# Optimization experiments

Hardware: AMD Instinct MI355X
Metric: run time of the kernel (lower is better)

The kernel has to match this reference:

```python
import jax, jax.numpy as jnp
import numpy as np

B, L, D, H = 2, 2048, 2048, 16
Dh = D // H
THETA = 500000.0


def _init_rope(dim, seq_len, n_heads):
    # Returns freqs_cis of shape (1, seq_len, 1, head_dim//2, 2) -> [..., 0]=cos, [..., 1]=sin
    hd = dim // n_heads
    inv_freqs = 1.0 / (THETA ** (jnp.arange(0, hd, 2, dtype=jnp.float32) / hd))
    t = jnp.arange(seq_len, dtype=jnp.float32)
    freqs = jnp.outer(t, inv_freqs).astype(jnp.float32)  # (L, hd/2)
    fc = jnp.stack([jnp.cos(freqs)[None, :, None, :],
                    jnp.sin(freqs)[None, :, None, :]], axis=3)  # (1, L, 1, 2, hd/2)
    return fc.transpose(0, 1, 2, 4, 3)  # (1, L, 1, hd/2, 2)


def _apply_rope(q, k, freqs_cis):
    def rotate(x):
        x2 = x.reshape(*x.shape[:-1], -1, 2)  # (B, L, H, Dh/2, 2)
        f = freqs_cis[:, :x.shape[1]]
        cos, sin = f[..., 0], f[..., 1]
        r = jnp.stack([x2[..., 0] * cos - x2[..., 1] * sin,
                       x2[..., 1] * cos + x2[..., 0] * sin], axis=-1)
        return r.reshape(*x.shape)
    return rotate(q), rotate(k)


def setup_inputs() -> dict:
    key = jax.random.key(0)
    kx, kq, kk, kv, ko = jax.random.split(key, 5)
    scale = 1.0 / np.sqrt(D)
    x = jax.random.normal(kx, (B, L, D), dtype=jnp.float32)
    Wq = jax.random.normal(kq, (D, H, Dh), dtype=jnp.float32) * scale
    Wk = jax.random.normal(kk, (D, H, Dh), dtype=jnp.float32) * scale
    Wv = jax.random.normal(kv, (D, H, Dh), dtype=jnp.float32) * scale
    Wo = jax.random.normal(ko, (D, D), dtype=jnp.float32) * scale
    return {"x": x, "Wq": Wq, "Wk": Wk, "Wv": Wv, "Wo": Wo}


def reference(x, Wq, Wk, Wv, Wo):
    freqs_cis = _init_rope(D, L, H)
    q = jnp.einsum('bld,dhk->blhk', x, Wq)  # (B, L, H, Dh)
    k = jnp.einsum('bld,dhk->blhk', x, Wk)
    v = jnp.einsum('bld,dhk->blhk', x, Wv)
    q, k = _apply_rope(q, k, freqs_cis)
    q = q / (Dh ** 0.5)
    att = jnp.einsum('bqhd,bkhd->bhqk', q, k)  # (B, H, L, L)
    Lq = x.shape[1]
    mask = jnp.tril(jnp.ones((1, 1, Lq, Lq), dtype=jnp.bool_))
    neg_inf = jnp.finfo(jnp.float32).min
    att = jnp.where(mask, att, neg_inf)
    att = jax.nn.softmax(att, axis=-1)
    out = jnp.einsum('bhqk,bkhd->bqhd', att, v)  # (B, L, H, Dh)
    out = out.reshape(x.shape)
    return jnp.einsum('bld,de->ble', out, Wo)
```

## Files before the change

### kernel.cpp

```cpp
#include <hip/hip_runtime.h>

typedef unsigned short u16;
typedef unsigned int u32;

#define Bb 2
#define Lc 2048
#define Dc 2048
#define Hc 16
#define DhC 128

typedef __bf16 bf16x8 __attribute__((ext_vector_type(8)));
typedef float f32x4 __attribute__((ext_vector_type(4)));

__device__ __forceinline__ u16 f2b(float f) {
  u32 u = __float_as_uint(f);
  u32 r = (u + 0x7fffu + ((u >> 16) & 1u)) >> 16;
  return (u16)r;
}
__device__ __forceinline__ float b2f(u16 u) {
  return __uint_as_float(((u32)u) << 16);
}

__device__ __forceinline__ void gll16(const void* g, void* l) {
  __builtin_amdgcn_global_load_lds(
      (const __attribute__((address_space(1))) u32*)g,
      (__attribute__((address_space(3))) u32*)l, 16, 0, 0);
}

__global__ __launch_bounds__(256) void sniff_dtype(const u16* __restrict__ x,
                                                   int* __restrict__ flag) {
  __shared__ int bad;
  if (threadIdx.x == 0) bad = 0;
  __syncthreads();
  int local = 0;
  for (int i = threadIdx.x; i < 65536; i += 256) {
    float v = fabsf(b2f(x[i]));
    if (!(v < 1000.f)) local = 1;
  }
  if (local) atomicOr(&bad, 1);
  __syncthreads();
  if (threadIdx.x == 0) *flag = bad;
}

__global__ __launch_bounds__(256) void conv_x(const void* __restrict__ in,
                                              u16* __restrict__ out,
                                              const int* __restrict__ flag) {
  const int f32 = *flag;
  const int i0 = (blockIdx.x * 256 + threadIdx.x) * 4;
  if (f32) {
    const float* p = (const float*)in;
#pragma unroll
    for (int j = 0; j < 4; j++) out[i0 + j] = f2b(p[i0 + j]);
  } else {
    const u16* p = (const u16*)in;
#pragma unroll
    for (int j = 0; j < 4; j++) out[i0 + j] = p[i0 + j];
  }
}

__global__ __launch_bounds__(256) void transpose2d_conv(const void* __restrict__ in,
                                                        u16* __restrict__ out,
                                                        const int* __restrict__ flag) {
  __shared__ __align__(16) u16 tile[64][65];
  const int f32 = *flag;
  const int r0 = blockIdx.y * 64, c0 = blockIdx.x * 64;
  const int tc = threadIdx.x & 63, tr4 = threadIdx.x >> 6;
#pragma unroll
  for (int p = 0; p < 16; p++) {
    int r = tr4 + p * 4;
    size_t idx = (size_t)(r0 + r) * 2048 + c0 + tc;
    tile[r][tc] = f32 ? f2b(((const float*)in)[idx]) : ((const u16*)in)[idx];
  }
  __syncthreads();
#pragma unroll
  for (int p = 0; p < 16; p++) {
    int rr = tr4 + p * 4;
    out[(size_t)(c0 + rr) * 2048 + r0 + tc] = tile[tc][rr];
  }
}

template <typename OutT>
__device__ __forceinline__ void gemm_bt_core(const u16* __restrict__ A,
                                             const u16* __restrict__ Bt,
                                             OutT* __restrict__ C) {
  constexpr int K = 2048, N = 2048;
  __shared__ __align__(16) u16 As[128 * 64];
  __shared__ __align__(16) u16 Bs[128 * 64];
  const int tid = threadIdx.x;
  const int lane = tid & 63, wid = tid >> 6;
  const int wm = (wid >> 1) * 64, wn = (wid & 1) * 64;
  const int m0 = blockIdx.x * 128, n0 = blockIdx.y * 128;
  const int quad = lane >> 4, l15 = lane & 15;
  const int sw = l15 & 7;

  const f32x4 fz = {0.f, 0.f, 0.f, 0.f};
  f32x4 acc[4][4];
#pragma unroll
  for (int i = 0; i < 4; i++)
#pragma unroll
    for (int j = 0; j < 4; j++) acc[i][j] = fz;

  const int srl = (lane >> 3);
  const int ssl = lane & 7;

  for (int k0 = 0; k0 < K; k0 += 64) {
#pragma unroll
    for (int p = 0; p < 4; p++) {
      const int r = p * 32 + wid * 8 + srl;
      const int c = ssl ^ (r & 7);
      u16* lb = As + (p * 256 + wid * 64) * 8;
      gll16(A + (size_t)(m0 + r) * K + k0 + c * 8, lb);
    }
#pragma unroll
    for (int p = 0; p < 4; p++) {
      const int r = p * 32 + wid * 8 + srl;
      const int c = ssl ^ (r & 7);
      u16* lb = Bs + (p * 256 + wid * 64) * 8;
      gll16(Bt + (size_t)(n0 + r) * K + k0 + c * 8, lb);
    }
    __syncthreads();
#pragma unroll
    for (int ks = 0; ks < 2; ks++) {
      bf16x8 af[4], bfr[4];
#pragma unroll
      for (int t = 0; t < 4; t++) {
        const int cc = ((ks * 4 + quad) ^ sw) * 8;
        af[t]  = *(const bf16x8*)(&As[(wm + t * 16 + l15) * 64 + cc]);
        bfr[t] = *(const bf16x8*)(&Bs[(wn + t * 16 + l15) * 64 + cc]);
      }
#pragma unroll
      for (int mt = 0; mt < 4; mt++)
#pragma unroll
        for (int nt = 0; nt < 4; nt++)
          acc[mt][nt] = __builtin_amdgcn_mfma_f32_16x16x32_bf16(af[mt], bfr[nt], acc[mt][nt], 0, 0, 0);
    }
    __syncthreads();
  }
#pragma unroll
  for (int mt = 0; mt < 4; mt++)
#pragma unroll
    for (int nt = 0; nt < 4; nt++) {
      int col = n0 + wn + nt * 16 + l15;
#pragma unroll
      for (int r = 0; r < 4; r++) {
        int row = m0 + wm + mt * 16 + quad * 4 + r;
        float v = acc[mt][nt][r];
        if constexpr (sizeof(OutT) == 2)
          C[(size_t)row * N + col] = f2b(v);
        else
          C[(size_t)row * N + col] = v;
      }
    }
}

__global__ __launch_bounds__(256) void gemm_bt(const u16* __restrict__ A,
                                               const u16* __restrict__ Bt,
                                               u16* __restrict__ C) {
  gemm_bt_core<u16>(A, Bt, C);
}
__global__ __launch_bounds__(256) void gemm_bt_f32(const u16* __restrict__ A,
                                                   const u16* __restrict__ Bt,
                                                   float* __restrict__ C) {
  gemm_bt_core<float>(A, Bt, C);
}

__global__ __launch_bounds__(256) void transpose_v_k(const u16* __restrict__ V,
                                                     u16* __restrict__ Vt) {
  __shared__ __align__(16) u16 tile[64][65];
  const int z = blockIdx.z;
  const int b = z >> 4, h = z & 15;
  const int l0 = blockIdx.y * 64, d0 = blockIdx.x * 64;
  const int tc = threadIdx.x & 63, tr4 = threadIdx.x >> 6;
#pragma unroll
  for (int p = 0; p < 16; p++) {
    int l = tr4 + p * 4;
    tile[l][tc] = V[(size_t)((b * Lc + l0 + l) * Hc + h) * DhC + d0 + tc];
  }
  __syncthreads();
#pragma unroll
  for (int p = 0; p < 16; p++) {
    int dd = tr4 + p * 4;
    Vt[((size_t)z * DhC + d0 + dd) * Lc + l0 + tc] = tile[tc][dd];
  }
}

__global__ __launch_bounds__(256) void rope_qk(u16* __restrict__ Q, u16* __restrict__ K) {
  const int idx = blockIdx.x * 256 + threadIdx.x;
  const int j = idx & 63;
  const int l = (idx >> 10) & 2047;
  const float inv = expf(-0.2050369278f * (float)j);
  const float ang = (float)l * inv;
  float s, c;
  sincosf(ang, &s, &c);
  const size_t off = (size_t)idx * 2;
  const float q0 = b2f(Q[off]), q1 = b2f(Q[off + 1]);
  const float k0 = b2f(K[off]), k1 = b2f(K[off + 1]);
  const float sc = 0.08838834764f;
  Q[off]     = f2b((q0 * c - q1 * s) * sc);
  Q[off + 1] = f2b((q1 * c + q0 * s) * sc);
  K[off]     = f2b(k0 * c - k1 * s);
  K[off + 1] = f2b(k1 * c + k0 * s);
}

#define NEGBIG (-3.0e30f)
__global__ __launch_bounds__(256) void flash_attn(const u16* __restrict__ Q,
                                                  const u16* __restrict__ Kg,
                                                  const u16* __restrict__ Vt,
                                                  u16* __restrict__ O) {
  __shared__ __align__(16) u16 Ks[2][64 * 128];
  __shared__ __align__(16) u16 Vs[2][128 * 64];
  __shared__ __align__(16) u16 Ps[4][16][72];
  const int tid = threadIdx.x;
  const int lane = tid & 63, w = tid >> 6;
  const int quad = lane >> 4, l15 = lane & 15;
  const int qt = (int)gridDim.x - 1 - (int)blockIdx.x;
  const int bh = blockIdx.y;
  const int b = bh >> 4, h = bh & 15;
  const int q0 = qt * 64;
  const int qrow = q0 + w * 16 + l15;

  const int krl = lane >> 4, ksl = lane & 15;
  const int vrl = lane >> 3, vsl = lane & 7;

  bf16x8 aq[4];
  const u16* qptr = Q + ((size_t)(b * Lc + qrow) * Hc + h) * DhC + quad * 8;
#pragma unroll
  for (int ks = 0; ks < 4; ks++) aq[ks] = *(const bf16x8*)(qptr + ks * 32);

  {
#pragma unroll
    for (int p = 0; p < 4; p++) {
      const int r = p * 16 + w * 4 + krl;
      const int c = ksl ^ (r & 15);
      gll16(Kg + ((size_t)(b * Lc + r) * Hc + h) * DhC + c * 8,
            &Ks[0][(p * 256 + w * 64) * 8]);
    }
#pragma unroll
    for (int p = 0; p < 4; p++) {
      const int r = p * 32 + w * 8 + vrl;
      const int c = vsl ^ (r & 7);
      gll16(Vt + ((size_t)bh * DhC + r) * Lc + c * 8,
            &Vs[0][(p * 256 + w * 64) * 8]);
    }
  }

  const f32x4 fz = {0.f, 0.f, 0.f, 0.f};
  f32x4 o[8];
#pragma unroll
  for (int f = 0; f < 8; f++) o[f] = fz;
  float mrow[4], lrow[4];
#pragma unroll
  for (int r = 0; r < 4; r++) { mrow[r] = NEGBIG; lrow[r] = 0.f; }

  __syncthreads();

  for (int kvt = 0; kvt <= qt; kvt++) {
    const int cur = kvt & 1;
    const u16* Ksc = Ks[cur];
    const u16* Vsc = Vs[cur];

    if (kvt < qt) {
      const int nv0 = (kvt + 1) * 64;
      const int nxt = cur ^ 1;
#pragma unroll
      for (int p = 0; p < 4; p++) {
        const int r = p * 16 + w * 4 + krl;
        const int c = ksl ^ (r & 15);
        gll16(Kg + ((size_t)(b * Lc + nv0 + r) * Hc + h) * DhC + c * 8,
              &Ks[nxt][(p * 256 + w * 64) * 8]);
      }
#pragma unroll
      for (int p = 0; p < 4; p++) {
        const int r = p * 32 + w * 8 + vrl;
        const int c = vsl ^ (r & 7);
        gll16(Vt + ((size_t)bh * DhC + r) * Lc + nv0 + c * 8,
              &Vs[nxt][(p * 256 + w * 64) * 8]);
      }
    }

    f32x4 s[4];
#pragma unroll
    for (int ct = 0; ct < 4; ct++) s[ct] = fz;
#pragma unroll
    for (int ks = 0; ks < 4; ks++) {
#pragma unroll
      for (int ct = 0; ct < 4; ct++) {
        bf16x8 bk = *(const bf16x8*)(
            &Ksc[(ct * 16 + l15) * 128 + (((ks << 2) + quad) ^ l15) * 8]);
        s[ct] = __builtin_amdgcn_mfma_f32_16x16x32_bf16(aq[ks], bk, s[ct], 0, 0, 0);
      }
    }

    if (kvt == qt) {
      const int kv0 = kvt * 64;
#pragma unroll
      for (int ct = 0; ct < 4; ct++) {
        int kvc = kv0 + ct * 16 + l15;
#pragma unroll
        for (int r = 0; r < 4; r++) {
          int qr = q0 + w * 16 + quad * 4 + r;
          if (kvc > qr) s[ct][r] = NEGBIG;
        }
      }
    }

    float mnew[4], alpha[4];
#pragma unroll
    for (int r = 0; r < 4; r++) {
      float mx = fmaxf(fmaxf(s[0][r], s[1][r]), fmaxf(s[2][r], s[3][r]));
#pragma unroll
      for (int off = 1; off < 16; off <<= 1) mx = fmaxf(mx, __shfl_xor(mx, off, 64));
      mnew[r] = fmaxf(mrow[r], mx);
      alpha[r] = __expf(mrow[r] - mnew[r]);
      mrow[r] = mnew[r];
    }
    float psum[4] = {0.f, 0.f, 0.f, 0.f};
#pragma unroll
    for (int ct = 0; ct < 4; ct++) {
#pragma unroll
      for (int r = 0; r < 4; r++) {
        float p = __expf(s[ct][r] - mnew[r]);
        s[ct][r] = p;
        psum[r] += p;
      }
    }
#pragma unroll
    for (int r = 0; r < 4; r++) {
#pragma unroll
      for (int off = 1; off < 16; off <<= 1) psum[r] += __shfl_xor(psum[r], off, 64);
      lrow[r] = lrow[r] * alpha[r] + psum[r];
    }
#pragma unroll
    for (int f = 0; f < 8; f++)
#pragma unroll
      for (int r = 0; r < 4; r++) o[f][r] *= alpha[r];

#pragma unroll
    for (int ct = 0; ct < 4; ct++)
#pragma unroll
      for (int r = 0; r < 4; r++)
        Ps[w][quad * 4 + r][ct * 16 + l15] = f2b(s[ct][r]);

#pragma unroll
    for (int ks = 0; ks < 2; ks++) {
      bf16x8 ap = *(const bf16x8*)(&Ps[w][l15][ks * 32 + quad * 8]);
#pragma unroll
      for (int f = 0; f < 8; f++) {
        bf16x8 bv = *(const bf16x8*)(
            &Vsc[(f * 16 + l15) * 64 + ((((ks << 2) + quad)) ^ (l15 & 7)) * 8]);
        o[f] = __builtin_amdgcn_mfma_f32_16x16x32_bf16(ap, bv, o[f], 0, 0, 0);
      }
    }

    __syncthreads();
  }

#pragma unroll
  for (int f = 0; f < 8; f++) {
    int d = f * 16 + l15;
#pragma unroll
    for (int r = 0; r < 4; r++) {
      int qr = q0 + w * 16 + quad * 4 + r;
      O[((size_t)(b * Lc + qr) * Hc + h) * DhC + d] = f2b(o[f][r] / lrow[r]);
    }
  }
}

extern "C" void kernel_launch(void* const* d_in, const int* in_sizes, int n_in,
                              void* d_out, int out_size, void* d_ws, size_t ws_size,
                              hipStream_t stream) {
  const void* x  = d_in[0];
  const void* Wq = d_in[1];
  const void* Wk = d_in[2];
  const void* Wv = d_in[3];
  const void* Wo = d_in[4];
  float* out = (float*)d_out;

  char* w = (char*)d_ws;
  const size_t WSZ = (size_t)2048 * 2048;
  const size_t XSZ = (size_t)Bb * Lc * Dc;
  int* flag = (int*)w;
  u16* WT  = (u16*)(w + 256);
  u16* xc  = WT + WSZ;
  u16* Qb  = xc + XSZ;
  u16* Kb  = Qb + XSZ;
  u16* Vb  = Kb + XSZ;
  u16* Vtb = xc;
  u16* Ob  = Vb;

  sniff_dtype<<<1, 256, 0, stream>>>((const u16*)x, flag);
  conv_x<<<(int)(XSZ / 1024), 256, 0, stream>>>(x, xc, flag);

  dim3 tgrid(32, 32);
  dim3 ggrid(32, 16);

  transpose2d_conv<<<tgrid, 256, 0, stream>>>(Wq, WT, flag);
  gemm_bt<<<ggrid, 256, 0, stream>>>(xc, WT, Qb);
  transpose2d_conv<<<tgrid, 256, 0, stream>>>(Wk, WT, flag);
  gemm_bt<<<ggrid, 256, 0, stream>>>(xc, WT, Kb);
  transpose2d_conv<<<tgrid, 256, 0, stream>>>(Wv, WT, flag);
  gemm_bt<<<ggrid, 256, 0, stream>>>(xc, WT, Vb);

  rope_qk<<<(Bb * Lc * Hc * 64) / 256, 256, 0, stream>>>(Qb, Kb);

  dim3 vgrid(2, 32, 32);
  transpose_v_k<<<vgrid, 256, 0, stream>>>(Vb, Vtb);

  dim3 fgrid(32, 32);
  flash_attn<<<fgrid, 256, 0, stream>>>(Qb, Kb, Vtb, Ob);

  transpose2d_conv<<<tgrid, 256, 0, stream>>>(Wo, WT, flag);
  gemm_bt_f32<<<ggrid, 256, 0, stream>>>(Ob, WT, out);
}
```

Measured before the change: 590.6 us.

## Rewrite flash attention with 32x32 MFMA, 128-row Q tiles and register P

Rewrites the flash attention kernel so each block handles 128 query rows and each wave 32 rows, switching to 32x32x16 MFMA with S computed transposed (K as A operand). P goes from accumulator to A-operand layout through lane shuffles and packed bf16 converts, so the LDS round trip is gone. It adds a lazy rescale that skips the output correction when the running max grows by no more than 8, s_setprio around the MFMA blocks, causal-balanced tile ordering across heads, and a launch-bounds occupancy hint. The aim is higher MFMA throughput, more K/V reuse per tile and less softmax and LDS overhead, at the cost of more registers and idle waves on diagonal tiles.

```diff
diff --git a/kernel.cpp b/kernel.cpp
--- a/kernel.cpp
+++ b/kernel.cpp
@@ -11,6 +11,7 @@
 
 typedef __bf16 bf16x8 __attribute__((ext_vector_type(8)));
 typedef float f32x4 __attribute__((ext_vector_type(4)));
+typedef float f32x16 __attribute__((ext_vector_type(16)));
 
 __device__ __forceinline__ u16 f2b(float f) {
   u32 u = __float_as_uint(f);
@@ -19,6 +20,12 @@
 }
 __device__ __forceinline__ float b2f(u16 u) {
   return __uint_as_float(((u32)u) << 16);
+}
+
+__device__ __forceinline__ u32 cvtpk(float lo, float hi) {
+  u32 r;
+  asm("v_cvt_pk_bf16_f32 %0, %1, %2" : "=v"(r) : "v"(lo), "v"(hi));
+  return r;
 }
 
 __device__ __forceinline__ void gll16(const void* g, void* l) {
@@ -203,29 +210,31 @@
 }
 
 #define NEGBIG (-3.0e30f)
-__global__ __launch_bounds__(256) void flash_attn(const u16* __restrict__ Q,
-                                                  const u16* __restrict__ Kg,
-                                                  const u16* __restrict__ Vt,
-                                                  u16* __restrict__ O) {
+__global__ __launch_bounds__(256, 2) void flash_attn(const u16* __restrict__ Q,
+                                                     const u16* __restrict__ Kg,
+                                                     const u16* __restrict__ Vt,
+                                                     u16* __restrict__ O) {
   __shared__ __align__(16) u16 Ks[2][64 * 128];
   __shared__ __align__(16) u16 Vs[2][128 * 64];
-  __shared__ __align__(16) u16 Ps[4][16][72];
   const int tid = threadIdx.x;
   const int lane = tid & 63, w = tid >> 6;
-  const int quad = lane >> 4, l15 = lane & 15;
-  const int qt = (int)gridDim.x - 1 - (int)blockIdx.x;
+  const int l31 = lane & 31, hib = lane >> 5;
   const int bh = blockIdx.y;
   const int b = bh >> 4, h = bh & 15;
-  const int q0 = qt * 64;
-  const int qrow = q0 + w * 16 + l15;
+  const int qt = (bh & 16) ? (int)blockIdx.x : (15 - (int)blockIdx.x);
+  const int q0 = qt * 128;
+  const int qw0 = q0 + w * 32;
+  const int nkv = 2 * qt + 2;
 
   const int krl = lane >> 4, ksl = lane & 15;
   const int vrl = lane >> 3, vsl = lane & 7;
 
-  bf16x8 aq[4];
-  const u16* qptr = Q + ((size_t)(b * Lc + qrow) * Hc + h) * DhC + quad * 8;
-#pragma unroll
-  for (int ks = 0; ks < 4; ks++) aq[ks] = *(const bf16x8*)(qptr + ks * 32);
+  bf16x8 qf[8];
+  {
+    const u16* qptr = Q + ((size_t)(b * Lc + qw0 + l31) * Hc + h) * DhC + 8 * hib;
+#pragma unroll
+    for (int s = 0; s < 8; s++) qf[s] = *(const bf16x8*)(qptr + s * 16);
+  }
 
   {
 #pragma unroll
@@ -244,22 +253,19 @@
     }
   }
 
-  const f32x4 fz = {0.f, 0.f, 0.f, 0.f};
-  f32x4 o[8];
-#pragma unroll
-  for (int f = 0; f < 8; f++) o[f] = fz;
-  float mrow[4], lrow[4];
-#pragma unroll
-  for (int r = 0; r < 4; r++) { mrow[r] = NEGBIG; lrow[r] = 0.f; }
+  f32x16 o[4];
+#pragma unroll
+  for (int dt = 0; dt < 4; dt++) o[dt] = (f32x16)0.0f;
+  float mrow = NEGBIG, lrow = 0.f;
 
   __syncthreads();
 
-  for (int kvt = 0; kvt <= qt; kvt++) {
+  for (int kvt = 0; kvt < nkv; kvt++) {
     const int cur = kvt & 1;
     const u16* Ksc = Ks[cur];
     const u16* Vsc = Vs[cur];
 
-    if (kvt < qt) {
+    if (kvt + 1 < nkv) {
       const int nv0 = (kvt + 1) * 64;
       const int nxt = cur ^ 1;
 #pragma unroll
@@ -278,91 +284,125 @@
       }
     }
 
-    f32x4 s[4];
-#pragma unroll
-    for (int ct = 0; ct < 4; ct++) s[ct] = fz;
-#pragma unroll
-    for (int ks = 0; ks < 4; ks++) {
-#pragma unroll
-      for (int ct = 0; ct < 4; ct++) {
-        bf16x8 bk = *(const bf16x8*)(
-            &Ksc[(ct * 16 + l15) * 128 + (((ks << 2) + quad) ^ l15) * 8]);
-        s[ct] = __builtin_amdgcn_mfma_f32_16x16x32_bf16(aq[ks], bk, s[ct], 0, 0, 0);
-      }
-    }
-
-    if (kvt == qt) {
-      const int kv0 = kvt * 64;
-#pragma unroll
-      for (int ct = 0; ct < 4; ct++) {
-        int kvc = kv0 + ct * 16 + l15;
-#pragma unroll
-        for (int r = 0; r < 4; r++) {
-          int qr = q0 + w * 16 + quad * 4 + r;
-          if (kvc > qr) s[ct][r] = NEGBIG;
+    const int kv0 = kvt * 64;
+    const bool active = (kv0 <= qw0 + 31);
+    if (active) {
+      f32x16 s0 = (f32x16)0.0f, s1 = (f32x16)0.0f;
+      __builtin_amdgcn_s_setprio(1);
+#pragma unroll
+      for (int s = 0; s < 8; s++) {
+        const int ch = ((2 * s + hib) ^ (l31 & 15)) * 8;
+        bf16x8 k0 = *(const bf16x8*)(&Ksc[l31 * 128 + ch]);
+        bf16x8 k1 = *(const bf16x8*)(&Ksc[(32 + l31) * 128 + ch]);
+        s0 = __builtin_amdgcn_mfma_f32_32x32x16_bf16(k0, qf[s], s0, 0, 0, 0);
+        s1 = __builtin_amdgcn_mfma_f32_32x32x16_bf16(k1, qf[s], s1, 0, 0, 0);
+      }
+      __builtin_amdgcn_s_setprio(0);
+
+      if (kv0 + 63 > qw0) {
+        const int qg = qw0 + l31;
+#pragma unroll
+        for (int r = 0; r < 16; r++) {
+          const int cr = (r & 3) + 8 * (r >> 2) + 4 * hib;
+          if (kv0 + cr > qg) s0[r] = NEGBIG;
+          if (kv0 + 32 + cr > qg) s1[r] = NEGBIG;
         }
       }
-    }
-
-    float mnew[4], alpha[4];
-#pragma unroll
-    for (int r = 0; r < 4; r++) {
-      float mx = fmaxf(fmaxf(s[0][r], s[1][r]), fmaxf(s[2][r], s[3][r]));
-#pragma unroll
-      for (int off = 1; off < 16; off <<= 1) mx = fmaxf(mx, __shfl_xor(mx, off, 64));
-      mnew[r] = fmaxf(mrow[r], mx);
-      alpha[r] = __expf(mrow[r] - mnew[r]);
-      mrow[r] = mnew[r];
-    }
-    float psum[4] = {0.f, 0.f, 0.f, 0.f};
-#pragma unroll
-    for (int ct = 0; ct < 4; ct++) {
-#pragma unroll
-      for (int r = 0; r < 4; r++) {
-        float p = __expf(s[ct][r] - mnew[r]);
-        s[ct][r] = p;
-        psum[r] += p;
-      }
-    }
-#pragma unroll
-    for (int r = 0; r < 4; r++) {
-#pragma unroll
-      for (int off = 1; off < 16; off <<= 1) psum[r] += __shfl_xor(psum[r], off, 64);
-      lrow[r] = lrow[r] * alpha[r] + psum[r];
-    }
-#pragma unroll
-    for (int f = 0; f < 8; f++)
-#pragma unroll
-      for (int r = 0; r < 4; r++) o[f][r] *= alpha[r];
-
-#pragma unroll
-    for (int ct = 0; ct < 4; ct++)
-#pragma unroll
-      for (int r = 0; r < 4; r++)
-        Ps[w][quad * 4 + r][ct * 16 + l15] = f2b(s[ct][r]);
-
-#pragma unroll
-    for (int ks = 0; ks < 2; ks++) {
-      bf16x8 ap = *(const bf16x8*)(&Ps[w][l15][ks * 32 + quad * 8]);
-#pragma unroll
-      for (int f = 0; f < 8; f++) {
-        bf16x8 bv = *(const bf16x8*)(
-            &Vsc[(f * 16 + l15) * 64 + ((((ks << 2) + quad)) ^ (l15 & 7)) * 8]);
-        o[f] = __builtin_amdgcn_mfma_f32_16x16x32_bf16(ap, bv, o[f], 0, 0, 0);
-      }
+
+      float mx;
+      {
+        float a[8];
+#pragma unroll
+        for (int i = 0; i < 8; i++)
+          a[i] = fmaxf(fmaxf(s0[i], s0[i + 8]), fmaxf(s1[i], s1[i + 8]));
+        float b0 = fmaxf(a[0], a[4]), b1 = fmaxf(a[1], a[5]);
+        float b2 = fmaxf(a[2], a[6]), b3 = fmaxf(a[3], a[7]);
+        mx = fmaxf(fmaxf(b0, b1), fmaxf(b2, b3));
+      }
+      mx = fmaxf(mx, __shfl_xor(mx, 32, 64));
+
+      if (!__all(mx - mrow <= 8.f)) {
+        const float mnew = fmaxf(mrow, mx);
+        const float al = __expf(mrow - mnew);
+#pragma unroll
+        for (int dt = 0; dt < 4; dt++)
+#pragma unroll
+          for (int e = 0; e < 16; e++) o[dt][e] *= al;
+        lrow *= al;
+        mrow = mnew;
+      }
+
+#pragma unroll
+      for (int i = 0; i < 16; i++) {
+        s0[i] = __expf(s0[i] - mrow);
+        s1[i] = __expf(s1[i] - mrow);
+      }
+      float sm;
+      {
+        float a[8];
+#pragma unroll
+        for (int i = 0; i < 8; i++)
+          a[i] = (s0[i] + s0[i + 8]) + (s1[i] + s1[i + 8]);
+        sm = ((a[0] + a[4]) + (a[1] + a[5])) + ((a[2] + a[6]) + (a[3] + a[7]));
+      }
+      sm += __shfl_xor(sm, 32, 64);
+      lrow += sm;
+
+      bf16x8 paf[4];
+#pragma unroll
+      for (int t = 0; t < 2; t++) {
+#pragma unroll
+        for (int h8 = 0; h8 < 2; h8++) {
+          const int rB = 8 * h8;
+          u32 lo0, lo1, hi0, hi1;
+          if (t == 0) {
+            lo0 = cvtpk(s0[rB + 0], s0[rB + 1]);
+            lo1 = cvtpk(s0[rB + 2], s0[rB + 3]);
+            hi0 = cvtpk(s0[rB + 4], s0[rB + 5]);
+            hi1 = cvtpk(s0[rB + 6], s0[rB + 7]);
+          } else {
+            lo0 = cvtpk(s1[rB + 0], s1[rB + 1]);
+            lo1 = cvtpk(s1[rB + 2], s1[rB + 3]);
+            hi0 = cvtpk(s1[rB + 4], s1[rB + 5]);
+            hi1 = cvtpk(s1[rB + 6], s1[rB + 7]);
+          }
+          const u32 g0 = hib ? lo0 : hi0;
+          const u32 g1 = hib ? lo1 : hi1;
+          const u32 r0 = (u32)__shfl_xor((int)g0, 32, 64);
+          const u32 r1 = (u32)__shfl_xor((int)g1, 32, 64);
+          union { u32 u[4]; bf16x8 v; } pu;
+          pu.u[0] = hib ? r0 : lo0;
+          pu.u[1] = hib ? r1 : lo1;
+          pu.u[2] = hib ? hi0 : r0;
+          pu.u[3] = hib ? hi1 : r1;
+          paf[2 * t + h8] = pu.v;
+        }
+      }
+
+      __builtin_amdgcn_s_setprio(1);
+#pragma unroll
+      for (int B = 0; B < 4; B++) {
+#pragma unroll
+        for (int dt = 0; dt < 4; dt++) {
+          const bf16x8 vf = *(const bf16x8*)(
+              &Vsc[(32 * dt + l31) * 64 + (((2 * B + hib) ^ (l31 & 7))) * 8]);
+          o[dt] = __builtin_amdgcn_mfma_f32_32x32x16_bf16(paf[B], vf, o[dt], 0, 0, 0);
+        }
+      }
+      __builtin_amdgcn_s_setprio(0);
     }
 
     __syncthreads();
   }
 
 #pragma unroll
-  for (int f = 0; f < 8; f++) {
-    int d = f * 16 + l15;
-#pragma unroll
-    for (int r = 0; r < 4; r++) {
-      int qr = q0 + w * 16 + quad * 4 + r;
-      O[((size_t)(b * Lc + qr) * Hc + h) * DhC + d] = f2b(o[f][r] / lrow[r]);
-    }
+  for (int r = 0; r < 16; r++) {
+    const int cr = (r & 3) + 8 * (r >> 2) + 4 * hib;
+    const float linv = 1.0f / __shfl(lrow, cr, 64);
+    const size_t rowoff = ((size_t)(b * Lc + qw0 + cr) * Hc + h) * DhC + l31;
+#pragma unroll
+    for (int dt = 0; dt < 4; dt++)
+      O[rowoff + 32 * dt] = f2b(o[dt][r] * linv);
   }
 }
 
@@ -406,7 +446,7 @@
   dim3 vgrid(2, 32, 32);
   transpose_v_k<<<vgrid, 256, 0, stream>>>(Vb, Vtb);
 
-  dim3 fgrid(32, 32);
+  dim3 fgrid(16, 32);
   flash_attn<<<fgrid, 256, 0, stream>>>(Qb, Kb, Vtb, Ob);
 
   transpose2d_conv<<<tgrid, 256, 0, stream>>>(Wo, WT, flag);
```

Measured after the change: 493.8 us. 1.2x faster.
